# Performance work log

Hardware: AMD Instinct MI355X
Metric: run time of the kernel (lower is better)

## Reference

```python
import jax, jax.numpy as jnp
import numpy as np

N = 10000      # nodes
E = 160000     # edges (avg degree 16)
D = 128        # channels
H = 4          # heads
C = 128        # per-head dim (PyG: out_channels per head = channels)
HC = H * C
EPS_SOFTMAX = 1e-16
EPS_NORM = 1e-5


def setup_inputs() -> dict:
    key = jax.random.key(0)
    ks = jax.random.split(key, 12)
    s = 1.0 / np.sqrt(D)
    sb = 1.0 / np.sqrt(3 * D)
    return {
        "x": jax.random.normal(ks[0], (N, D), jnp.float32),
        "edge_index": jax.random.randint(ks[1], (2, E), 0, N, dtype=jnp.int64),
        "Wq": jax.random.normal(ks[2], (D, HC), jnp.float32) * s,
        "bq": jnp.zeros((HC,), jnp.float32),
        "Wk": jax.random.normal(ks[3], (D, HC), jnp.float32) * s,
        "bk": jnp.zeros((HC,), jnp.float32),
        "Wv": jax.random.normal(ks[4], (D, HC), jnp.float32) * s,
        "bv": jnp.zeros((HC,), jnp.float32),
        "Wskip": jax.random.normal(ks[5], (D, D), jnp.float32) * s,
        "bskip": jnp.zeros((D,), jnp.float32),
        "Wbeta": jax.random.normal(ks[6], (3 * D,), jnp.float32) * sb,  # lin_beta, bias=False
        "gn_weight": jnp.ones((D,), jnp.float32),
        "gn_bias": jnp.zeros((D,), jnp.float32),
        "gn_mean_scale": jnp.ones((D,), jnp.float32),
    }


def reference(x, edge_index, Wq, bq, Wk, bk, Wv, bv, Wskip, bskip, Wbeta,
              gn_weight, gn_bias, gn_mean_scale):
    n = x.shape[0]
    src, dst = edge_index[0], edge_index[1]  # messages flow src(j) -> dst(i)

    # Projections [N,H,C]
    q = (x @ Wq + bq).reshape(n, H, C)
    k = (x @ Wk + bk).reshape(n, H, C)
    v = (x @ Wv + bv).reshape(n, H, C)

    # Per-edge attention logits [E,H]
    alpha = jnp.einsum('ehc,ehc->eh', q[dst], k[src]) / jnp.sqrt(jnp.float32(C))

    # Segment softmax over incoming edges of each dst node
    amax = jax.ops.segment_max(alpha, dst, num_segments=n)       # [N,H]
    amax = jnp.where(jnp.isfinite(amax), amax, 0.0)
    ex = jnp.exp(alpha - amax[dst])                              # [E,H]
    denom = jax.ops.segment_sum(ex, dst, num_segments=n)         # [N,H]
    attn = ex / (denom[dst] + EPS_SOFTMAX)                       # [E,H]

    # Weighted scatter-aggregate, then mean over heads (concat=False)
    msgs = attn[:, :, None] * v[src]                             # [E,H,C]
    out = jax.ops.segment_sum(msgs, dst, num_segments=n)         # [N,H,C]
    out = out.mean(axis=1)                                       # [N,D]

    # Beta-gated skip (PyG: beta = sigmoid(lin_beta([out, x_r, out - x_r])))
    skip = x @ Wskip + bskip
    beta = jax.nn.sigmoid(jnp.concatenate([out, skip, out - skip], axis=-1) @ Wbeta)
    beta = beta[:, None]
    out = beta * skip + (1.0 - beta) * out

    # GraphNorm (single graph): (x - mean_scale*mean) / sqrt(var + eps) * w + b
    mean = out.mean(axis=0)
    centered = out - gn_mean_scale * mean
    var = (centered * centered).mean(axis=0)
    out = gn_weight * centered / jnp.sqrt(var + EPS_NORM) + gn_bias

    # GELU (exact) + residual (shapes match); dropout is identity in eval
    out = jax.nn.gelu(out, approximate=False)
    return out + x
```

## Files before the change

### kernel.cpp

```cpp
#include <hip/hip_runtime.h>
#include <hip/hip_bf16.h>
#include <math.h>

#define D_DIM 128
#define HC_DIM 512
#define CAP 128
#define REP 4

typedef __attribute__((ext_vector_type(8))) short bf16x8;
typedef __attribute__((ext_vector_type(4))) float f32x4;
typedef __attribute__((ext_vector_type(2))) float f32x2;
typedef __attribute__((ext_vector_type(2))) _Float16 h16x2;

static __device__ __forceinline__ unsigned short f2bf(float f) {
  unsigned u = __float_as_uint(f);
  unsigned r = (u + 0x7fffu + ((u >> 16) & 1u)) >> 16;
  return (unsigned short)r;
}
static __device__ __forceinline__ float bflo(unsigned u) {
  return __uint_as_float(u << 16);
}
static __device__ __forceinline__ float bfhi(unsigned u) {
  return __uint_as_float(u & 0xffff0000u);
}

__global__ void prep_kernel(const float* __restrict__ x,
                            const float* __restrict__ Wq, const float* __restrict__ Wk,
                            const float* __restrict__ Wv, const float* __restrict__ Wskip,
                            const float* __restrict__ bq, const float* __restrict__ bk,
                            const float* __restrict__ bv, const float* __restrict__ bskip,
                            unsigned short* __restrict__ xb,
                            unsigned short* __restrict__ wcat,
                            float* __restrict__ bcat,
                            int* __restrict__ zbase, int zwords, int N) {
  int t = blockIdx.x * 256 + threadIdx.x;
  int X4 = N * 32;
  if (t < X4) {
    float4 f = *(const float4*)&x[t * 4];
    ushort4 o;
    o.x = f2bf(f.x); o.y = f2bf(f.y); o.z = f2bf(f.z); o.w = f2bf(f.w);
    *(ushort4*)&xb[t * 4] = o;
  } else if (t < X4 + 1664 * 128) {
    int widx = t - X4;
    if (widx < 3 * 65536) {
      int segi = widx >> 16;
      int r = widx & 65535;
      int kk = r >> 9;
      int m = r & 511;
      const float* W = (segi == 0) ? Wq : (segi == 1) ? Wk : Wv;
      wcat[(size_t)(segi * 512 + m) * 128 + kk] = f2bf(W[kk * 512 + m]);
    } else {
      int r = widx - 3 * 65536;
      int kk = r >> 7;
      int m = r & 127;
      wcat[(size_t)(1536 + m) * 128 + kk] = f2bf(Wskip[kk * 128 + m]);
    }
  } else if (t < X4 + 1664 * 128 + 1664) {
    int b = t - X4 - 1664 * 128;
    bcat[b] = (b < 512) ? bq[b] : (b < 1024) ? bk[b - 512]
            : (b < 1536) ? bv[b - 1024] : bskip[b - 1536];
  } else if (t < X4 + 1664 * 128 + 1664 + zwords) {
    zbase[t - X4 - 1664 * 128 - 1664] = 0;
  }
}

__global__ __launch_bounds__(256) void gemm_mfma_kernel(
    const unsigned short* __restrict__ Xb, const unsigned short* __restrict__ Wt,
    const float* __restrict__ bcat, unsigned short* __restrict__ qb,
    unsigned char* __restrict__ k8, unsigned char* __restrict__ v8,
    float* __restrict__ skip,
    const int* __restrict__ src, const int* __restrict__ dst,
    int* __restrict__ cnt, int* __restrict__ bsrc, int N, int E) {
  const int tid = threadIdx.x;
  {
    int nblk = gridDim.x * gridDim.y;
    int lb = blockIdx.y * gridDim.x + blockIdx.x;
    int per = (E + nblk - 1) / nblk;
    int e0 = lb * per;
    int e1 = min(e0 + per, E);
    for (int e = e0 + tid; e < e1; e += 256) {
      int d = dst[e];
      int p = atomicAdd(&cnt[d], 1);
      if (p < CAP) bsrc[d * CAP + p] = src[e];
    }
  }
  const int wave = tid >> 6, lane = tid & 63;
  const int l16 = lane & 15, quad = lane >> 4;
  const int row0 = (blockIdx.x * 4 + wave) * 64;
  const int col0 = blockIdx.y * 64;

  const unsigned short* xrow[4];
#pragma unroll
  for (int i = 0; i < 4; ++i) {
    int r = row0 + i * 16 + l16;
    if (r >= N) r = N - 1;
    xrow[i] = Xb + (size_t)r * 128;
  }
  const unsigned short* wrow[4];
  float bias[4];
#pragma unroll
  for (int j = 0; j < 4; ++j) {
    int c = col0 + j * 16 + l16;
    wrow[j] = Wt + (size_t)c * 128;
    bias[j] = bcat[c];
  }

  f32x4 acc[4][4] = {};
#pragma unroll
  for (int kk = 0; kk < 4; ++kk) {
    int k0 = kk * 32 + quad * 8;
    bf16x8 a[4], b[4];
#pragma unroll
    for (int i = 0; i < 4; ++i) a[i] = *(const bf16x8*)(xrow[i] + k0);
#pragma unroll
    for (int j = 0; j < 4; ++j) b[j] = *(const bf16x8*)(wrow[j] + k0);
#pragma unroll
    for (int i = 0; i < 4; ++i)
#pragma unroll
      for (int j = 0; j < 4; ++j)
        acc[i][j] = __builtin_amdgcn_mfma_f32_16x16x32_bf16(a[i], b[j], acc[i][j], 0, 0, 0);
  }

  const int kind = (col0 < 512) ? 0 : (col0 < 1024) ? 1 : (col0 < 1536) ? 2 : 3;
#pragma unroll
  for (int i = 0; i < 4; ++i) {
#pragma unroll
    for (int reg = 0; reg < 4; ++reg) {
      int r = row0 + i * 16 + quad * 4 + reg;
      if (r < N) {
#pragma unroll
        for (int j = 0; j < 4; ++j) {
          int cidx = col0 + j * 16 + l16;
          float val = acc[i][j][reg] + bias[j];
          if (kind == 0) {
            qb[(size_t)r * 512 + cidx] = f2bf(val);
          } else if (kind == 1) {
            int pk = __builtin_amdgcn_cvt_pk_fp8_f32(val, val, 0, false);
            k8[(size_t)r * 512 + cidx - 512] = (unsigned char)pk;
          } else if (kind == 2) {
            int pk = __builtin_amdgcn_cvt_pk_fp8_f32(val, val, 0, false);
            v8[(size_t)r * 512 + cidx - 1024] = (unsigned char)pk;
          } else {
            skip[(size_t)r * 128 + cidx - 1536] = val;
          }
        }
      }
    }
  }
}

__global__ __launch_bounds__(256) void attn_combine_kernel(
    const unsigned short* __restrict__ qb, const unsigned char* __restrict__ k8,
    const unsigned char* __restrict__ v8, const int* __restrict__ cnt,
    const int* __restrict__ bsrc, const float* __restrict__ skip,
    const float* __restrict__ Wbeta, float* __restrict__ out2,
    float* __restrict__ colsum, float* __restrict__ colsq, int N) {
  __shared__ int eL[4][CAP];
  __shared__ float redS[4][128];
  __shared__ float redQ[4][128];
  int tid = threadIdx.x;
  int w = tid >> 6, lane = tid & 63;
  int node = blockIdx.x * 4 + w;
  bool nv = node < N;
  int nc = nv ? node : (N - 1);
  int g = lane >> 4, j = lane & 15;

  int count = nv ? min(cnt[nc], CAP) : 0;
  const int* bp = bsrc + (size_t)nc * CAP;
  for (int i = lane; i < count; i += 64) eL[w][i] = bp[i];

  const float qscale = 0.08838834764831845f * 1.4426950408889634f;
  float qf[4][8];
#pragma unroll
  for (int h = 0; h < 4; ++h) {
    int4 qi = *(const int4*)(qb + (size_t)nc * 512 + h * 128 + j * 8);
    qf[h][0] = bflo(qi.x) * qscale; qf[h][1] = bfhi(qi.x) * qscale;
    qf[h][2] = bflo(qi.y) * qscale; qf[h][3] = bfhi(qi.y) * qscale;
    qf[h][4] = bflo(qi.z) * qscale; qf[h][5] = bfhi(qi.z) * qscale;
    qf[h][6] = bflo(qi.w) * qscale; qf[h][7] = bfhi(qi.w) * qscale;
  }

  float o[4][8];
  float lsum[4];
#pragma unroll
  for (int h = 0; h < 4; ++h) {
    lsum[h] = 0.f;
#pragma unroll
    for (int r = 0; r < 8; ++r) o[h][r] = 0.f;
  }

  if (count > 0) {
    int e = eL[w][(g < count) ? g : 0];
    uint2 kw[4]; uint2 vw[4];
    {
      const unsigned char* kbe = k8 + (size_t)e * 512 + j * 8;
      const unsigned char* vbe = v8 + (size_t)e * 512 + j * 8;
#pragma unroll
      for (int h = 0; h < 4; ++h) {
        kw[h] = *(const uint2*)(kbe + h * 128);
        vw[h] = *(const uint2*)(vbe + h * 128);
      }
    }
    for (int idx = 0; idx < count; idx += 4) {
      int rem = count - idx;
      int nrem = rem - 4;
      int en = (nrem > 0) ? eL[w][idx + 4 + ((g < nrem) ? g : 0)] : e;
      uint2 kwn[4]; uint2 vwn[4];
      {
        const unsigned char* kbe = k8 + (size_t)en * 512 + j * 8;
        const unsigned char* vbe = v8 + (size_t)en * 512 + j * 8;
#pragma unroll
        for (int h = 0; h < 4; ++h) {
          kwn[h] = *(const uint2*)(kbe + h * 128);
          vwn[h] = *(const uint2*)(vbe + h * 128);
        }
      }
      bool act = (g < rem);
#pragma unroll
      for (int h = 0; h < 4; ++h) {
        f32x2 k01 = __builtin_amdgcn_cvt_pk_f32_fp8(kw[h].x, false);
        f32x2 k23 = __builtin_amdgcn_cvt_pk_f32_fp8(kw[h].x, true);
        f32x2 k45 = __builtin_amdgcn_cvt_pk_f32_fp8(kw[h].y, false);
        f32x2 k67 = __builtin_amdgcn_cvt_pk_f32_fp8(kw[h].y, true);
        float p = qf[h][0] * k01.x;
        p = fmaf(qf[h][1], k01.y, p);
        p = fmaf(qf[h][2], k23.x, p);
        p = fmaf(qf[h][3], k23.y, p);
        p = fmaf(qf[h][4], k45.x, p);
        p = fmaf(qf[h][5], k45.y, p);
        p = fmaf(qf[h][6], k67.x, p);
        p = fmaf(qf[h][7], k67.y, p);
        p += __shfl_xor(p, 1);
        p += __shfl_xor(p, 2);
        p += __shfl_xor(p, 4);
        p += __shfl_xor(p, 8);
        float a = act ? p : -1e30f;
        float wgt = exp2f(a);
        f32x2 v01 = __builtin_amdgcn_cvt_pk_f32_fp8(vw[h].x, false);
        f32x2 v23 = __builtin_amdgcn_cvt_pk_f32_fp8(vw[h].x, true);
        f32x2 v45 = __builtin_amdgcn_cvt_pk_f32_fp8(vw[h].y, false);
        f32x2 v67 = __builtin_amdgcn_cvt_pk_f32_fp8(vw[h].y, true);
        lsum[h] += wgt;
        o[h][0] += wgt * v01.x; o[h][1] += wgt * v01.y;
        o[h][2] += wgt * v23.x; o[h][3] += wgt * v23.y;
        o[h][4] += wgt * v45.x; o[h][5] += wgt * v45.y;
        o[h][6] += wgt * v67.x; o[h][7] += wgt * v67.y;
        kw[h] = kwn[h]; vw[h] = vwn[h];
      }
      e = en;
    }
  }
  float am[8];
#pragma unroll
  for (int r = 0; r < 8; ++r) am[r] = 0.f;
#pragma unroll
  for (int h = 0; h < 4; ++h) {
#pragma unroll
    for (int r = 0; r < 8; ++r) {
      o[h][r] += __shfl_xor(o[h][r], 16);
      o[h][r] += __shfl_xor(o[h][r], 32);
    }
    lsum[h] += __shfl_xor(lsum[h], 16);
    lsum[h] += __shfl_xor(lsum[h], 32);
    float inv = 0.25f / (lsum[h] + 1e-16f);
#pragma unroll
    for (int r = 0; r < 8; ++r) am[r] += o[h][r] * inv;
  }

  float4 sl = *(const float4*)&skip[(size_t)nc * 128 + j * 8];
  float4 sh = *(const float4*)&skip[(size_t)nc * 128 + j * 8 + 4];
  float4 wal = *(const float4*)&Wbeta[j * 8];
  float4 wah = *(const float4*)&Wbeta[j * 8 + 4];
  float4 wbl = *(const float4*)&Wbeta[128 + j * 8];
  float4 wbh = *(const float4*)&Wbeta[128 + j * 8 + 4];
  float4 wcl = *(const float4*)&Wbeta[256 + j * 8];
  float4 wch = *(const float4*)&Wbeta[256 + j * 8 + 4];
  float p = am[0] * wal.x + sl.x * wbl.x + (am[0] - sl.x) * wcl.x
          + am[1] * wal.y + sl.y * wbl.y + (am[1] - sl.y) * wcl.y
          + am[2] * wal.z + sl.z * wbl.z + (am[2] - sl.z) * wcl.z
          + am[3] * wal.w + sl.w * wbl.w + (am[3] - sl.w) * wcl.w
          + am[4] * wah.x + sh.x * wbh.x + (am[4] - sh.x) * wch.x
          + am[5] * wah.y + sh.y * wbh.y + (am[5] - sh.y) * wch.y
          + am[6] * wah.z + sh.z * wbh.z + (am[6] - sh.z) * wch.z
          + am[7] * wah.w + sh.w * wbh.w + (am[7] - sh.w) * wch.w;
  p += __shfl_xor(p, 1); p += __shfl_xor(p, 2);
  p += __shfl_xor(p, 4); p += __shfl_xor(p, 8);
  float beta = 1.f / (1.f + __expf(-p));
  float ob = 1.f - beta;
  float vm = nv ? 1.f : 0.f;
  float oc0 = (beta * sl.x + ob * am[0]) * vm;
  float oc1 = (beta * sl.y + ob * am[1]) * vm;
  float oc2 = (beta * sl.z + ob * am[2]) * vm;
  float oc3 = (beta * sl.w + ob * am[3]) * vm;
  float oc4 = (beta * sh.x + ob * am[4]) * vm;
  float oc5 = (beta * sh.y + ob * am[5]) * vm;
  float oc6 = (beta * sh.z + ob * am[6]) * vm;
  float oc7 = (beta * sh.w + ob * am[7]) * vm;

  if (g == 0) {
    float4 lo; lo.x = oc0; lo.y = oc1; lo.z = oc2; lo.w = oc3;
    float4 hi; hi.x = oc4; hi.y = oc5; hi.z = oc6; hi.w = oc7;
    if (nv) {
      *(float4*)&out2[(size_t)node * 128 + j * 8] = lo;
      *(float4*)&out2[(size_t)node * 128 + j * 8 + 4] = hi;
    }
    *(float4*)&redS[w][j * 8] = lo;
    *(float4*)&redS[w][j * 8 + 4] = hi;
    float4 ql; ql.x = oc0 * oc0; ql.y = oc1 * oc1; ql.z = oc2 * oc2; ql.w = oc3 * oc3;
    float4 qh2; qh2.x = oc4 * oc4; qh2.y = oc5 * oc5; qh2.z = oc6 * oc6; qh2.w = oc7 * oc7;
    *(float4*)&redQ[w][j * 8] = ql;
    *(float4*)&redQ[w][j * 8 + 4] = qh2;
  }
  __syncthreads();
  if (w == 0) {
    int c = lane * 2;
    float s0 = redS[0][c] + redS[1][c] + redS[2][c] + redS[3][c];
    float s1 = redS[0][c + 1] + redS[1][c + 1] + redS[2][c + 1] + redS[3][c + 1];
    float q0 = redQ[0][c] + redQ[1][c] + redQ[2][c] + redQ[3][c];
    float q1 = redQ[0][c + 1] + redQ[1][c + 1] + redQ[2][c + 1] + redQ[3][c + 1];
    int slot = (blockIdx.x & (REP - 1)) * 128;
    atomicAdd(&colsum[slot + c], s0);
    atomicAdd(&colsum[slot + c + 1], s1);
    atomicAdd(&colsq[slot + c], q0);
    atomicAdd(&colsq[slot + c + 1], q1);
  }
}

__global__ void final_kernel(const float* __restrict__ out2,
                             const float* __restrict__ colsum,
                             const float* __restrict__ colsq,
                             const float* __restrict__ gnw,
                             const float* __restrict__ gnb,
                             const float* __restrict__ gnms,
                             const float* __restrict__ x,
                             float* __restrict__ y, int total2, float invN) {
  int i = blockIdx.x * 256 + threadIdx.x;
  if (i < total2) {
    int c = (i & 63) * 2;
    float2 cs; cs.x = 0.f; cs.y = 0.f;
    float2 cq; cq.x = 0.f; cq.y = 0.f;
#pragma unroll
    for (int s = 0; s < REP; ++s) {
      float2 t = *(const float2*)&colsum[s * 128 + c];
      float2 u = *(const float2*)&colsq[s * 128 + c];
      cs.x += t.x; cs.y += t.y;
      cq.x += u.x; cq.y += u.y;
    }
    float2 gw = *(const float2*)&gnw[c];
    float2 gb = *(const float2*)&gnb[c];
    float2 gs = *(const float2*)&gnms[c];
    float mean0 = cs.x * invN, mean1 = cs.y * invN;
    float var0 = cq.x * invN - mean0 * mean0 * gs.x * (2.f - gs.x);
    float var1 = cq.y * invN - mean1 * mean1 * gs.y * (2.f - gs.y);
    float mul0 = gw.x / sqrtf(var0 + 1e-5f);
    float mul1 = gw.y / sqrtf(var1 + 1e-5f);
    float2 o = *(const float2*)&out2[i * 2];
    float2 xx = *(const float2*)&x[i * 2];
    float t0 = (o.x - gs.x * mean0) * mul0 + gb.x;
    float t1 = (o.y - gs.y * mean1) * mul1 + gb.y;
    float g0 = 0.5f * t0 * (1.f + erff(t0 * 0.70710678118654752f));
    float g1 = 0.5f * t1 * (1.f + erff(t1 * 0.70710678118654752f));
    float2 r; r.x = g0 + xx.x; r.y = g1 + xx.y;
    *(float2*)&y[i * 2] = r;
  }
}

extern "C" void kernel_launch(void* const* d_in, const int* in_sizes, int n_in,
                              void* d_out, int out_size, void* d_ws, size_t ws_size,
                              hipStream_t stream) {
  const float* x     = (const float*)d_in[0];
  const int*   ei    = (const int*)d_in[1];
  const float* Wq    = (const float*)d_in[2];
  const float* bq    = (const float*)d_in[3];
  const float* Wk    = (const float*)d_in[4];
  const float* bk    = (const float*)d_in[5];
  const float* Wv    = (const float*)d_in[6];
  const float* bv    = (const float*)d_in[7];
  const float* Wskip = (const float*)d_in[8];
  const float* bskip = (const float*)d_in[9];
  const float* Wbeta = (const float*)d_in[10];
  const float* gnw   = (const float*)d_in[11];
  const float* gnb   = (const float*)d_in[12];
  const float* gnms  = (const float*)d_in[13];

  const int N = in_sizes[0] / D_DIM;
  const int E = in_sizes[1] / 2;
  const int* src = ei;
  const int* dst = ei + E;

  char* p = (char*)d_ws;
  unsigned short* qb = (unsigned short*)p; p += (size_t)N * 512 * 2;
  unsigned char*  k8 = (unsigned char*)p;  p += (size_t)N * 512;
  unsigned char*  v8 = (unsigned char*)p;  p += (size_t)N * 512;
  float*          skip = (float*)p;        p += (size_t)N * 128 * 4;
  float*          out2 = (float*)p;        p += (size_t)N * 128 * 4;
  int*   cnt    = (int*)p;   p += (size_t)N * 4;
  float* colsum = (float*)p; p += REP * 128 * 4;
  float* colsq  = (float*)p; p += REP * 128 * 4;
  int zwords = N + 2 * REP * 128;
  int* bsrc   = (int*)p;   p += (size_t)N * CAP * 4;
  unsigned short* wcat = (unsigned short*)p; p += (size_t)1664 * 128 * 2;
  float* bcat = (float*)p; p += 1664 * 4;
  unsigned short* xb = (unsigned short*)out2;

  int prepTotal = N * 32 + 1664 * 128 + 1664 + zwords;
  prep_kernel<<<(prepTotal + 255) / 256, 256, 0, stream>>>(
      x, Wq, Wk, Wv, Wskip, bq, bk, bv, bskip, xb, wcat, bcat, cnt, zwords, N);

  gemm_mfma_kernel<<<dim3(40, 26), 256, 0, stream>>>(
      xb, wcat, bcat, qb, k8, v8, skip, src, dst, cnt, bsrc, N, E);

  attn_combine_kernel<<<(N + 3) / 4, 256, 0, stream>>>(
      qb, k8, v8, cnt, bsrc, skip, Wbeta, out2, colsum, colsq, N);

  int total2 = N * D_DIM / 2;
  final_kernel<<<(total2 + 255) / 256, 256, 0, stream>>>(
      out2, colsum, colsq, gnw, gnb, gnms, x, (float*)d_out, total2, 1.f / (float)N);
}
```

Baseline: 180.0 us.

## Stage gathered fp8 K/V rows into LDS via global_load_lds chunks

Replaces the register double-buffered per-edge K/V gathers with chunked direct global-to-LDS loads (16 bytes per lane, two edges per wave instruction), then computes attention from LDS. It aims for wider, better-coalesced gather transactions. In exchange it adds a full vmcnt wait per chunk, so loads and compute no longer overlap, and it uses 32KB of extra LDS per block, which may lower occupancy.

```diff
diff --git a/kernel.cpp b/kernel.cpp
--- a/kernel.cpp
+++ b/kernel.cpp
@@ -6,11 +6,11 @@
 #define HC_DIM 512
 #define CAP 128
 #define REP 4
+#define CHUNK 8
 
 typedef __attribute__((ext_vector_type(8))) short bf16x8;
 typedef __attribute__((ext_vector_type(4))) float f32x4;
 typedef __attribute__((ext_vector_type(2))) float f32x2;
-typedef __attribute__((ext_vector_type(2))) _Float16 h16x2;
 
 static __device__ __forceinline__ unsigned short f2bf(float f) {
   unsigned u = __float_as_uint(f);
@@ -22,6 +22,12 @@
 }
 static __device__ __forceinline__ float bfhi(unsigned u) {
   return __uint_as_float(u & 0xffff0000u);
+}
+
+static __device__ __forceinline__ void gload_lds16(const void* g, void* l) {
+  __builtin_amdgcn_global_load_lds(
+      (const __attribute__((address_space(1))) unsigned int*)g,
+      (__attribute__((address_space(3))) unsigned int*)l, 16, 0, 0);
 }
 
 __global__ void prep_kernel(const float* __restrict__ x,
@@ -158,6 +164,7 @@
   __shared__ int eL[4][CAP];
   __shared__ float redS[4][128];
   __shared__ float redQ[4][128];
+  __shared__ __align__(16) unsigned char kvL[4][2][CHUNK][512];
   int tid = threadIdx.x;
   int w = tid >> 6, lane = tid & 63;
   int node = blockIdx.x * 4 + w;
@@ -190,64 +197,61 @@
   }
 
   if (count > 0) {
-    int e = eL[w][(g < count) ? g : 0];
-    uint2 kw[4]; uint2 vw[4];
-    {
-      const unsigned char* kbe = k8 + (size_t)e * 512 + j * 8;
-      const unsigned char* vbe = v8 + (size_t)e * 512 + j * 8;
-#pragma unroll
-      for (int h = 0; h < 4; ++h) {
-        kw[h] = *(const uint2*)(kbe + h * 128);
-        vw[h] = *(const uint2*)(vbe + h * 128);
+    int half = lane >> 5;
+    int b16 = (lane & 31) * 16;
+    for (int base = 0; base < count; base += CHUNK) {
+      int m = min(CHUNK, count - base);
+      for (int t = 0; 2 * t < m; ++t) {
+        int ce = base + 2 * t + half;
+        int ei = eL[w][(ce < count) ? ce : (count - 1)];
+        const unsigned char* gk = k8 + (size_t)ei * 512 + b16;
+        const unsigned char* gv = v8 + (size_t)ei * 512 + b16;
+        gload_lds16(gk, &kvL[w][0][2 * t][0]);
+        gload_lds16(gv, &kvL[w][1][2 * t][0]);
       }
-    }
-    for (int idx = 0; idx < count; idx += 4) {
-      int rem = count - idx;
-      int nrem = rem - 4;
-      int en = (nrem > 0) ? eL[w][idx + 4 + ((g < nrem) ? g : 0)] : e;
-      uint2 kwn[4]; uint2 vwn[4];
-      {
-        const unsigned char* kbe = k8 + (size_t)en * 512 + j * 8;
-        const unsigned char* vbe = v8 + (size_t)en * 512 + j * 8;
+      asm volatile("s_waitcnt vmcnt(0)" ::: "memory");
+      __builtin_amdgcn_sched_barrier(0);
+      for (int s = 0; s < CHUNK && s < m; s += 4) {
+        int cl = s + g;
+        bool act = cl < m;
+        int clc = act ? cl : (m - 1);
+        const unsigned char* kp = &kvL[w][0][clc][0];
+        const unsigned char* vp = &kvL[w][1][clc][0];
 #pragma unroll
         for (int h = 0; h < 4; ++h) {
-          kwn[h] = *(const uint2*)(kbe + h * 128);
-          vwn[h] = *(const uint2*)(vbe + h * 128);
+          uint2 kw = *(const uint2*)(kp + h * 128 + j * 8);
+          uint2 vw = *(const uint2*)(vp + h * 128 + j * 8);
+          f32x2 k01 = __builtin_amdgcn_cvt_pk_f32_fp8(kw.x, false);
+          f32x2 k23 = __builtin_amdgcn_cvt_pk_f32_fp8(kw.x, true);
+          f32x2 k45 = __builtin_amdgcn_cvt_pk_f32_fp8(kw.y, false);
+          f32x2 k67 = __builtin_amdgcn_cvt_pk_f32_fp8(kw.y, true);
+          float p = qf[h][0] * k01.x;
+          p = fmaf(qf[h][1], k01.y, p);
+          p = fmaf(qf[h][2], k23.x, p);
+          p = fmaf(qf[h][3], k23.y, p);
+          p = fmaf(qf[h][4], k45.x, p);
+          p = fmaf(qf[h][5], k45.y, p);
+          p = fmaf(qf[h][6], k67.x, p);
+          p = fmaf(qf[h][7], k67.y, p);
+          p += __shfl_xor(p, 1);
+          p += __shfl_xor(p, 2);
+          p += __shfl_xor(p, 4);
+          p += __shfl_xor(p, 8);
+          float a = act ? p : -1e30f;
+          float wgt = exp2f(a);
+          f32x2 v01 = __builtin_amdgcn_cvt_pk_f32_fp8(vw.x, false);
+          f32x2 v23 = __builtin_amdgcn_cvt_pk_f32_fp8(vw.x, true);
+          f32x2 v45 = __builtin_amdgcn_cvt_pk_f32_fp8(vw.y, false);
+          f32x2 v67 = __builtin_amdgcn_cvt_pk_f32_fp8(vw.y, true);
+          lsum[h] += wgt;
+          o[h][0] = fmaf(wgt, v01.x, o[h][0]); o[h][1] = fmaf(wgt, v01.y, o[h][1]);
+          o[h][2] = fmaf(wgt, v23.x, o[h][2]); o[h][3] = fmaf(wgt, v23.y, o[h][3]);
+          o[h][4] = fmaf(wgt, v45.x, o[h][4]); o[h][5] = fmaf(wgt, v45.y, o[h][5]);
+          o[h][6] = fmaf(wgt, v67.x, o[h][6]); o[h][7] = fmaf(wgt, v67.y, o[h][7]);
         }
       }
-      bool act = (g < rem);
-#pragma unroll
-      for (int h = 0; h < 4; ++h) {
-        f32x2 k01 = __builtin_amdgcn_cvt_pk_f32_fp8(kw[h].x, false);
-        f32x2 k23 = __builtin_amdgcn_cvt_pk_f32_fp8(kw[h].x, true);
-        f32x2 k45 = __builtin_amdgcn_cvt_pk_f32_fp8(kw[h].y, false);
-        f32x2 k67 = __builtin_amdgcn_cvt_pk_f32_fp8(kw[h].y, true);
-        float p = qf[h][0] * k01.x;
-        p = fmaf(qf[h][1], k01.y, p);
-        p = fmaf(qf[h][2], k23.x, p);
-        p = fmaf(qf[h][3], k23.y, p);
-        p = fmaf(qf[h][4], k45.x, p);
-        p = fmaf(qf[h][5], k45.y, p);
-        p = fmaf(qf[h][6], k67.x, p);
-        p = fmaf(qf[h][7], k67.y, p);
-        p += __shfl_xor(p, 1);
-        p += __shfl_xor(p, 2);
-        p += __shfl_xor(p, 4);
-        p += __shfl_xor(p, 8);
-        float a = act ? p : -1e30f;
-        float wgt = exp2f(a);
-        f32x2 v01 = __builtin_amdgcn_cvt_pk_f32_fp8(vw[h].x, false);
-        f32x2 v23 = __builtin_amdgcn_cvt_pk_f32_fp8(vw[h].x, true);
-        f32x2 v45 = __builtin_amdgcn_cvt_pk_f32_fp8(vw[h].y, false);
-        f32x2 v67 = __builtin_amdgcn_cvt_pk_f32_fp8(vw[h].y, true);
-        lsum[h] += wgt;
-        o[h][0] += wgt * v01.x; o[h][1] += wgt * v01.y;
-        o[h][2] += wgt * v23.x; o[h][3] += wgt * v23.y;
-        o[h][4] += wgt * v45.x; o[h][5] += wgt * v45.y;
-        o[h][6] += wgt * v67.x; o[h][7] += wgt * v67.y;
-        kw[h] = kwn[h]; vw[h] = vwn[h];
-      }
-      e = en;
+      asm volatile("s_waitcnt lgkmcnt(0)" ::: "memory");
+      __builtin_amdgcn_sched_barrier(0);
     }
   }
   float am[8];
```

Result: slower. 184.9 us (+2.7%).
